# Kernel optimization log

Hardware: AMD Instinct MI355X
Metric: run time of the kernel (lower is better)

## Reference

```python
import jax, jax.numpy as jnp
import numpy as np
from jax import lax

PS = 8  # patch size

def setup_inputs() -> dict:
    key = jax.random.key(0)
    ks = jax.random.split(key, 7)
    dim = 64
    B, H, W = 4, 256, 256
    x = jax.random.normal(ks[0], (B, dim, H, W), dtype=jnp.float32)
    # to_hidden: Conv2d(dim, 6*dim, k=1)
    w_hidden = jax.random.normal(ks[1], (6 * dim, dim, 1, 1), dtype=jnp.float32) * 0.05
    b_hidden = jax.random.normal(ks[2], (6 * dim,), dtype=jnp.float32) * 0.01
    # to_hidden_dw: depthwise Conv2d(6*dim, 6*dim, k=3, pad=1, groups=6*dim)
    w_dw = jax.random.normal(ks[3], (6 * dim, 1, 3, 3), dtype=jnp.float32) * 0.05
    b_dw = jax.random.normal(ks[4], (6 * dim,), dtype=jnp.float32) * 0.01
    # project_out: Conv2d(2*dim, dim, k=1)
    w_out = jax.random.normal(ks[5], (dim, 2 * dim, 1, 1), dtype=jnp.float32) * 0.05
    b_out = jax.random.normal(ks[6], (dim,), dtype=jnp.float32) * 0.01
    return {"x": x, "w_hidden": w_hidden, "b_hidden": b_hidden,
            "w_dw": w_dw, "b_dw": b_dw, "w_out": w_out, "b_out": b_out}

def _conv(x, w, groups=1, padding='VALID'):
    return lax.conv_general_dilated(
        x, w, window_strides=(1, 1), padding=padding,
        dimension_numbers=('NCHW', 'OIHW', 'NCHW'),
        feature_group_count=groups)

def reference(x, w_hidden, b_hidden, w_dw, b_dw, w_out, b_out):
    # 1x1 expansion to 6*dim channels
    hidden = _conv(x, w_hidden) + b_hidden[None, :, None, None]
    # 3x3 depthwise conv (groups == channels)
    dw = _conv(hidden, w_dw, groups=w_dw.shape[0], padding='SAME') + b_dw[None, :, None, None]
    q, k, v = jnp.split(dw, 3, axis=1)  # each (B, 2*dim, H, W)
    B, C, H, W = q.shape
    # raw reshape into (B,C,H/8,W/8,8,8) exactly as torch .reshape on contiguous NCHW
    q_patch = q.reshape(B, C, H // PS, W // PS, PS, PS)
    k_patch = k.reshape(B, C, H // PS, W // PS, PS, PS)
    q_fft = jnp.fft.rfft2(q_patch)
    k_fft = jnp.fft.rfft2(k_patch)
    out = jnp.fft.irfft2(q_fft * k_fft, s=(PS, PS))  # circular conv of q,k patches
    out = out.reshape(B, C, (H // PS) * PS, (W // PS) * PS)
    output = v * out
    output = _conv(output, w_out) + b_out[None, :, None, None]
    return output
```

## Files before the change

kernel.cpp:

```cpp
#include <hip/hip_runtime.h>

#define HW 65536
#define W_IMG 256
#define H_IMG 256
#define CIN 64
#define CHID 384
#define CQK 128

__global__ __launch_bounds__(256) void k1_expand(
    const float* __restrict__ x_base,
    const float* __restrict__ wh,
    const float* __restrict__ bh,
    float* __restrict__ hidden_base,
    size_t x_bstride, size_t hid_bstride)
{
    const float* x = x_base + blockIdx.z * x_bstride;
    float* hidden  = hidden_base + blockIdx.z * hid_bstride;
    const int pxbase = blockIdx.x * 256;
    const int cobase = blockIdx.y * 64;
    const int tid  = threadIdx.x;
    const int lane = tid & 63;
    const int wq   = __builtin_amdgcn_readfirstlane(tid >> 6);
    const int px   = pxbase + lane * 4;
    const int cw   = cobase + wq * 16;

    float acc[16][4];
    #pragma unroll
    for (int i = 0; i < 16; ++i)
        #pragma unroll
        for (int j = 0; j < 4; ++j) acc[i][j] = 0.f;

    #pragma unroll 2
    for (int ci4 = 0; ci4 < CIN; ci4 += 4) {
        float4 xv[4];
        #pragma unroll
        for (int u = 0; u < 4; ++u)
            xv[u] = *reinterpret_cast<const float4*>(&x[(size_t)(ci4 + u) * HW + px]);
        #pragma unroll
        for (int i = 0; i < 16; ++i) {
            float4 wv = *reinterpret_cast<const float4*>(
                &wh[(size_t)(cw + i) * CIN + ci4]);
            float wu[4] = {wv.x, wv.y, wv.z, wv.w};
            #pragma unroll
            for (int u = 0; u < 4; ++u) {
                acc[i][0] += wu[u] * xv[u].x;
                acc[i][1] += wu[u] * xv[u].y;
                acc[i][2] += wu[u] * xv[u].z;
                acc[i][3] += wu[u] * xv[u].w;
            }
        }
    }

    #pragma unroll
    for (int i = 0; i < 16; ++i) {
        int co = cw + i;
        float b = bh[co];
        float4 o;
        o.x = acc[i][0] + b; o.y = acc[i][1] + b;
        o.z = acc[i][2] + b; o.w = acc[i][3] + b;
        *reinterpret_cast<float4*>(&hidden[(size_t)co * HW + px]) = o;
    }
}

__global__ __launch_bounds__(256) void k2_fused(
    const float* __restrict__ hidden_base,
    const float* __restrict__ wdw,
    const float* __restrict__ bdw,
    float* __restrict__ vout_base,
    size_t hid_bstride, size_t vout_bstride)
{
    __shared__ float stg[2][10][260];
    __shared__ float qk[2][8][4][68];

    const float* hidden = hidden_base + blockIdx.z * hid_bstride;
    float* vout         = vout_base + blockIdx.z * vout_bstride;

    const int c  = blockIdx.y;
    const int r0 = blockIdx.x * 8;
    const int tid = threadIdx.x;

    #pragma unroll
    for (int it = 0; it < 5; ++it) {
        int f4  = it * 256 + tid;
        int ch  = f4 / 640;
        int rem = f4 - ch * 640;
        int lr  = rem >> 6;
        int p4  = rem & 63;
        int gr  = r0 - 1 + lr;
        float4 v = make_float4(0.f, 0.f, 0.f, 0.f);
        if ((unsigned)gr < H_IMG)
            v = *reinterpret_cast<const float4*>(
                &hidden[(size_t)(c + ch * CQK) * HW + (size_t)gr * W_IMG + p4 * 4]);
        *reinterpret_cast<float4*>(&stg[ch][lr][p4 * 4]) = v;
    }
    __syncthreads();

    const int w = tid;
    const int segw = w >> 6;
    const int tw   = w & 63;
    #pragma unroll
    for (int ch = 0; ch < 2; ++ch) {
        const float* wv = wdw + (c + ch * CQK) * 9;
        const float bias = bdw[c + ch * CQK];
        const float w0 = wv[0], w1 = wv[1], w2 = wv[2];
        const float w3 = wv[3], w4 = wv[4], w5 = wv[5];
        const float w6 = wv[6], w7 = wv[7], w8 = wv[8];
        const float* S = &stg[ch][0][0];

        float am, a0, ap, bm, b0, bp;
        a0 = S[w];
        am = (w > 0)   ? S[w - 1] : 0.f;
        ap = (w < 255) ? S[w + 1] : 0.f;
        b0 = S[260 + w];
        bm = (w > 0)   ? S[260 + w - 1] : 0.f;
        bp = (w < 255) ? S[260 + w + 1] : 0.f;

        #pragma unroll
        for (int r = 0; r < 8; ++r) {
            const float* Sr = S + (r + 2) * 260;
            float c0 = Sr[w];
            float cm = (w > 0)   ? Sr[w - 1] : 0.f;
            float cp = (w < 255) ? Sr[w + 1] : 0.f;
            float a = bias + am * w0 + a0 * w1 + ap * w2
                           + bm * w3 + b0 * w4 + bp * w5
                           + cm * w6 + c0 * w7 + cp * w8;
            qk[ch][r][segw][tw] = a;
            am = bm; a0 = b0; ap = bp;
            bm = cm; b0 = c0; bp = cp;
        }
    }
    __syncthreads();

    const int row = tid >> 5;
    const int seg = (tid >> 3) & 3;
    const int i   = tid & 7;
    const int gr  = r0 + row;
    const int wp0 = seg * 64 + i * 8;

    const float* hbv = hidden + (size_t)(c + 2 * CQK) * HW;
    float4 hv[3][2];
    float  hm[3], hp[3];
    #pragma unroll
    for (int ky = 0; ky < 3; ++ky) {
        int grr = gr + ky - 1;
        hv[ky][0] = make_float4(0.f, 0.f, 0.f, 0.f);
        hv[ky][1] = make_float4(0.f, 0.f, 0.f, 0.f);
        hm[ky] = 0.f; hp[ky] = 0.f;
        if ((unsigned)grr < H_IMG) {
            const float* rb = hbv + (size_t)grr * W_IMG;
            hv[ky][0] = *reinterpret_cast<const float4*>(&rb[wp0]);
            hv[ky][1] = *reinterpret_cast<const float4*>(&rb[wp0 + 4]);
            hm[ky] = (wp0 > 0)   ? rb[wp0 - 1] : 0.f;
            hp[ky] = (wp0 < 248) ? rb[wp0 + 8] : 0.f;
        }
    }

    const float* qb = &qk[0][row][seg][0];
    const float* kb = &qk[1][row][seg][0];

    float acc[8];
    #pragma unroll
    for (int j = 0; j < 8; ++j) acc[j] = 0.f;

    #pragma unroll
    for (int s = 0; s < 8; ++s) {
        int qr = (i - s) & 7;
        float4 ka = *reinterpret_cast<const float4*>(&kb[s * 8]);
        float4 kc = *reinterpret_cast<const float4*>(&kb[s * 8 + 4]);
        float4 qa = *reinterpret_cast<const float4*>(&qb[qr * 8]);
        float4 qc = *reinterpret_cast<const float4*>(&qb[qr * 8 + 4]);
        float kr[8] = {ka.x, ka.y, ka.z, ka.w, kc.x, kc.y, kc.z, kc.w};
        float qv[8] = {qa.x, qa.y, qa.z, qa.w, qc.x, qc.y, qc.z, qc.w};
        #pragma unroll
        for (int t = 0; t < 8; ++t)
            #pragma unroll
            for (int j = 0; j < 8; ++j)
                acc[j] += kr[t] * qv[(j - t) & 7];
    }

    const float* wvv = wdw + (c + 2 * CQK) * 9;
    const float vbias = bdw[c + 2 * CQK];
    float vc[8];
    #pragma unroll
    for (int j = 0; j < 8; ++j) vc[j] = vbias;
    #pragma unroll
    for (int ky = 0; ky < 3; ++ky) {
        float kw0 = wvv[ky * 3], kw1 = wvv[ky * 3 + 1], kw2 = wvv[ky * 3 + 2];
        float h[10];
        h[0] = hm[ky];
        h[1] = hv[ky][0].x; h[2] = hv[ky][0].y; h[3] = hv[ky][0].z; h[4] = hv[ky][0].w;
        h[5] = hv[ky][1].x; h[6] = hv[ky][1].y; h[7] = hv[ky][1].z; h[8] = hv[ky][1].w;
        h[9] = hp[ky];
        #pragma unroll
        for (int j = 0; j < 8; ++j)
            vc[j] += h[j] * kw0 + h[j + 1] * kw1 + h[j + 2] * kw2;
    }

    float* dst = &vout[(size_t)c * HW + (size_t)gr * W_IMG + wp0];
    float4 o0, o1;
    o0.x = acc[0] * vc[0]; o0.y = acc[1] * vc[1];
    o0.z = acc[2] * vc[2]; o0.w = acc[3] * vc[3];
    o1.x = acc[4] * vc[4]; o1.y = acc[5] * vc[5];
    o1.z = acc[6] * vc[6]; o1.w = acc[7] * vc[7];
    *reinterpret_cast<float4*>(dst)     = o0;
    *reinterpret_cast<float4*>(dst + 4) = o1;
}

__global__ __launch_bounds__(256) void k3_project(
    const float* __restrict__ vout_base,
    const float* __restrict__ wo,
    const float* __restrict__ bo,
    float* __restrict__ out_base,
    size_t vout_bstride, size_t out_bstride)
{
    const float* vout = vout_base + blockIdx.z * vout_bstride;
    float* out        = out_base + blockIdx.z * out_bstride;
    const int pxbase = blockIdx.x * 256;
    const int tid  = threadIdx.x;
    const int lane = tid & 63;
    const int wq   = __builtin_amdgcn_readfirstlane(tid >> 6);
    const int px   = pxbase + lane * 4;
    const int cw   = wq * 16;

    float acc[16][4];
    #pragma unroll
    for (int i = 0; i < 16; ++i)
        #pragma unroll
        for (int j = 0; j < 4; ++j) acc[i][j] = 0.f;

    #pragma unroll 2
    for (int cc4 = 0; cc4 < CQK; cc4 += 4) {
        float4 xv[4];
        #pragma unroll
        for (int u = 0; u < 4; ++u)
            xv[u] = *reinterpret_cast<const float4*>(&vout[(size_t)(cc4 + u) * HW + px]);
        #pragma unroll
        for (int i = 0; i < 16; ++i) {
            float4 wv = *reinterpret_cast<const float4*>(
                &wo[(size_t)(cw + i) * CQK + cc4]);
            float wu[4] = {wv.x, wv.y, wv.z, wv.w};
            #pragma unroll
            for (int u = 0; u < 4; ++u) {
                acc[i][0] += wu[u] * xv[u].x;
                acc[i][1] += wu[u] * xv[u].y;
                acc[i][2] += wu[u] * xv[u].z;
                acc[i][3] += wu[u] * xv[u].w;
            }
        }
    }

    #pragma unroll
    for (int i = 0; i < 16; ++i) {
        int co = cw + i;
        float b = bo[co];
        float4 o;
        o.x = acc[i][0] + b; o.y = acc[i][1] + b;
        o.z = acc[i][2] + b; o.w = acc[i][3] + b;
        *reinterpret_cast<float4*>(&out[(size_t)co * HW + px]) = o;
    }
}

extern "C" void kernel_launch(void* const* d_in, const int* in_sizes, int n_in,
                              void* d_out, int out_size, void* d_ws, size_t ws_size,
                              hipStream_t stream) {
    const float* x   = (const float*)d_in[0];
    const float* wh  = (const float*)d_in[1];
    const float* bh  = (const float*)d_in[2];
    const float* wdw = (const float*)d_in[3];
    const float* bdw = (const float*)d_in[4];
    const float* wo  = (const float*)d_in[5];
    const float* bo  = (const float*)d_in[6];
    float* out = (float*)d_out;

    const size_t n_hid  = (size_t)CHID * HW;
    const size_t n_vout = (size_t)CQK * HW;
    const size_t n_x    = (size_t)CIN * HW;

    if (ws_size >= 4 * (n_hid + n_vout) * sizeof(float)) {
        float* hidden = (float*)d_ws;
        float* vout   = hidden + 4 * n_hid;
        k1_expand <<<dim3(HW / 256, CHID / 64, 4), 256, 0, stream>>>(
            x, wh, bh, hidden, n_x, n_hid);
        k2_fused  <<<dim3(H_IMG / 8, CQK, 4),      256, 0, stream>>>(
            hidden, wdw, bdw, vout, n_hid, n_vout);
        k3_project<<<dim3(HW / 256, 1, 4),         256, 0, stream>>>(
            vout, wo, bo, out, n_vout, n_x);
    } else {
        float* hidden = (float*)d_ws;
        float* vout   = hidden + n_hid;
        for (int b = 0; b < 4; ++b) {
            const float* xb = x + (size_t)b * n_x;
            float* ob       = out + (size_t)b * n_x;
            k1_expand <<<dim3(HW / 256, CHID / 64, 1), 256, 0, stream>>>(
                xb, wh, bh, hidden, 0, 0);
            k2_fused  <<<dim3(H_IMG / 8, CQK, 1),      256, 0, stream>>>(
                hidden, wdw, bdw, vout, 0, 0);
            k3_project<<<dim3(HW / 256, 1, 1),         256, 0, stream>>>(
                vout, wo, bo, ob, 0, 0);
        }
    }
}
```

Before: 420.1 us.

## Shrink channel tiles in 1x1 convs and restage depthwise conv one channel at a time

k1_expand now computes 32 output channels per block instead of 64, and k3_project splits its 64 outputs across four blocks of 16. Both changes raise the block count and cut per-thread accumulator registers, which should help occupancy. The price is re-reading the input pixels more times. k2_fused now stages one q/k channel at a time into a smaller padded shared buffer with zero halo columns, which removes the boundary branches, and it issues the v-halo loads before the depthwise stage. This lowers LDS use but adds a sync between the two channels.

Result: faster. 407.5 us (-3.0%).

```diff
diff --git a/kernel.cpp b/kernel.cpp
--- a/kernel.cpp
+++ b/kernel.cpp
@@ -17,16 +17,16 @@
     const float* x = x_base + blockIdx.z * x_bstride;
     float* hidden  = hidden_base + blockIdx.z * hid_bstride;
     const int pxbase = blockIdx.x * 256;
-    const int cobase = blockIdx.y * 64;
+    const int cobase = blockIdx.y * 32;
     const int tid  = threadIdx.x;
     const int lane = tid & 63;
     const int wq   = __builtin_amdgcn_readfirstlane(tid >> 6);
     const int px   = pxbase + lane * 4;
-    const int cw   = cobase + wq * 16;
-
-    float acc[16][4];
-    #pragma unroll
-    for (int i = 0; i < 16; ++i)
+    const int cw   = cobase + wq * 8;
+
+    float acc[8][4];
+    #pragma unroll
+    for (int i = 0; i < 8; ++i)
         #pragma unroll
         for (int j = 0; j < 4; ++j) acc[i][j] = 0.f;
 
@@ -37,7 +37,7 @@
         for (int u = 0; u < 4; ++u)
             xv[u] = *reinterpret_cast<const float4*>(&x[(size_t)(ci4 + u) * HW + px]);
         #pragma unroll
-        for (int i = 0; i < 16; ++i) {
+        for (int i = 0; i < 8; ++i) {
             float4 wv = *reinterpret_cast<const float4*>(
                 &wh[(size_t)(cw + i) * CIN + ci4]);
             float wu[4] = {wv.x, wv.y, wv.z, wv.w};
@@ -52,7 +52,7 @@
     }
 
     #pragma unroll
-    for (int i = 0; i < 16; ++i) {
+    for (int i = 0; i < 8; ++i) {
         int co = cw + i;
         float b = bh[co];
         float4 o;
@@ -69,7 +69,7 @@
     float* __restrict__ vout_base,
     size_t hid_bstride, size_t vout_bstride)
 {
-    __shared__ float stg[2][10][260];
+    __shared__ float stg[10 * 264];
     __shared__ float qk[2][8][4][68];
 
     const float* hidden = hidden_base + blockIdx.z * hid_bstride;
@@ -78,58 +78,6 @@
     const int c  = blockIdx.y;
     const int r0 = blockIdx.x * 8;
     const int tid = threadIdx.x;
-
-    #pragma unroll
-    for (int it = 0; it < 5; ++it) {
-        int f4  = it * 256 + tid;
-        int ch  = f4 / 640;
-        int rem = f4 - ch * 640;
-        int lr  = rem >> 6;
-        int p4  = rem & 63;
-        int gr  = r0 - 1 + lr;
-        float4 v = make_float4(0.f, 0.f, 0.f, 0.f);
-        if ((unsigned)gr < H_IMG)
-            v = *reinterpret_cast<const float4*>(
-                &hidden[(size_t)(c + ch * CQK) * HW + (size_t)gr * W_IMG + p4 * 4]);
-        *reinterpret_cast<float4*>(&stg[ch][lr][p4 * 4]) = v;
-    }
-    __syncthreads();
-
-    const int w = tid;
-    const int segw = w >> 6;
-    const int tw   = w & 63;
-    #pragma unroll
-    for (int ch = 0; ch < 2; ++ch) {
-        const float* wv = wdw + (c + ch * CQK) * 9;
-        const float bias = bdw[c + ch * CQK];
-        const float w0 = wv[0], w1 = wv[1], w2 = wv[2];
-        const float w3 = wv[3], w4 = wv[4], w5 = wv[5];
-        const float w6 = wv[6], w7 = wv[7], w8 = wv[8];
-        const float* S = &stg[ch][0][0];
-
-        float am, a0, ap, bm, b0, bp;
-        a0 = S[w];
-        am = (w > 0)   ? S[w - 1] : 0.f;
-        ap = (w < 255) ? S[w + 1] : 0.f;
-        b0 = S[260 + w];
-        bm = (w > 0)   ? S[260 + w - 1] : 0.f;
-        bp = (w < 255) ? S[260 + w + 1] : 0.f;
-
-        #pragma unroll
-        for (int r = 0; r < 8; ++r) {
-            const float* Sr = S + (r + 2) * 260;
-            float c0 = Sr[w];
-            float cm = (w > 0)   ? Sr[w - 1] : 0.f;
-            float cp = (w < 255) ? Sr[w + 1] : 0.f;
-            float a = bias + am * w0 + a0 * w1 + ap * w2
-                           + bm * w3 + b0 * w4 + bp * w5
-                           + cm * w6 + c0 * w7 + cp * w8;
-            qk[ch][r][segw][tw] = a;
-            am = bm; a0 = b0; ap = bp;
-            bm = cm; b0 = c0; bp = cp;
-        }
-    }
-    __syncthreads();
 
     const int row = tid >> 5;
     const int seg = (tid >> 3) & 3;
@@ -155,6 +103,56 @@
         }
     }
 
+    const int w = tid;
+    const int segw = w >> 6;
+    const int tw   = w & 63;
+
+    #pragma unroll
+    for (int ch = 0; ch < 2; ++ch) {
+        if (ch) __syncthreads();
+        #pragma unroll
+        for (int it = 0; it < 3; ++it) {
+            int f4 = it * 256 + tid;
+            if (f4 < 640) {
+                int lr = f4 >> 6;
+                int p4 = f4 & 63;
+                int grr = r0 - 1 + lr;
+                float4 v = make_float4(0.f, 0.f, 0.f, 0.f);
+                if ((unsigned)grr < H_IMG)
+                    v = *reinterpret_cast<const float4*>(
+                        &hidden[(size_t)(c + ch * CQK) * HW + (size_t)grr * W_IMG + p4 * 4]);
+                *reinterpret_cast<float4*>(&stg[lr * 264 + 4 + p4 * 4]) = v;
+            }
+        }
+        if (tid < 10) {
+            stg[tid * 264 + 3]   = 0.f;
+            stg[tid * 264 + 260] = 0.f;
+        }
+        __syncthreads();
+
+        const float* wv = wdw + (c + ch * CQK) * 9;
+        const float bias = bdw[c + ch * CQK];
+        const float w0 = wv[0], w1 = wv[1], w2 = wv[2];
+        const float w3 = wv[3], w4 = wv[4], w5 = wv[5];
+        const float w6 = wv[6], w7 = wv[7], w8 = wv[8];
+
+        const float* S0 = &stg[w + 3];
+        float am = S0[0],       a0 = S0[1],       ap = S0[2];
+        float bm = S0[264],     b0 = S0[265],     bp = S0[266];
+        #pragma unroll
+        for (int r = 0; r < 8; ++r) {
+            const float* Sr = S0 + (r + 2) * 264;
+            float cm = Sr[0], c0 = Sr[1], cp = Sr[2];
+            float a = bias + am * w0 + a0 * w1 + ap * w2
+                           + bm * w3 + b0 * w4 + bp * w5
+                           + cm * w6 + c0 * w7 + cp * w8;
+            qk[ch][r][segw][tw] = a;
+            am = bm; a0 = b0; ap = bp;
+            bm = cm; b0 = c0; bp = cp;
+        }
+    }
+    __syncthreads();
+
     const float* qb = &qk[0][row][seg][0];
     const float* kb = &qk[1][row][seg][0];
 
@@ -216,15 +214,16 @@
     const float* vout = vout_base + blockIdx.z * vout_bstride;
     float* out        = out_base + blockIdx.z * out_bstride;
     const int pxbase = blockIdx.x * 256;
+    const int cobase = blockIdx.y * 16;
     const int tid  = threadIdx.x;
     const int lane = tid & 63;
     const int wq   = __builtin_amdgcn_readfirstlane(tid >> 6);
     const int px   = pxbase + lane * 4;
-    const int cw   = wq * 16;
-
-    float acc[16][4];
-    #pragma unroll
-    for (int i = 0; i < 16; ++i)
+    const int cw   = cobase + wq * 4;
+
+    float acc[4][4];
+    #pragma unroll
+    for (int i = 0; i < 4; ++i)
         #pragma unroll
         for (int j = 0; j < 4; ++j) acc[i][j] = 0.f;
 
@@ -235,7 +234,7 @@
         for (int u = 0; u < 4; ++u)
             xv[u] = *reinterpret_cast<const float4*>(&vout[(size_t)(cc4 + u) * HW + px]);
         #pragma unroll
-        for (int i = 0; i < 16; ++i) {
+        for (int i = 0; i < 4; ++i) {
             float4 wv = *reinterpret_cast<const float4*>(
                 &wo[(size_t)(cw + i) * CQK + cc4]);
             float wu[4] = {wv.x, wv.y, wv.z, wv.w};
@@ -250,7 +249,7 @@
     }
 
     #pragma unroll
-    for (int i = 0; i < 16; ++i) {
+    for (int i = 0; i < 4; ++i) {
         int co = cw + i;
         float b = bo[co];
         float4 o;
@@ -279,11 +278,11 @@
     if (ws_size >= 4 * (n_hid + n_vout) * sizeof(float)) {
         float* hidden = (float*)d_ws;
         float* vout   = hidden + 4 * n_hid;
-        k1_expand <<<dim3(HW / 256, CHID / 64, 4), 256, 0, stream>>>(
+        k1_expand <<<dim3(HW / 256, CHID / 32, 4), 256, 0, stream>>>(
             x, wh, bh, hidden, n_x, n_hid);
         k2_fused  <<<dim3(H_IMG / 8, CQK, 4),      256, 0, stream>>>(
             hidden, wdw, bdw, vout, n_hid, n_vout);
-        k3_project<<<dim3(HW / 256, 1, 4),         256, 0, stream>>>(
+        k3_project<<<dim3(HW / 256, 64 / 16, 4),   256, 0, stream>>>(
             vout, wo, bo, out, n_vout, n_x);
     } else {
         float* hidden = (float*)d_ws;
@@ -291,11 +290,11 @@
         for (int b = 0; b < 4; ++b) {
             const float* xb = x + (size_t)b * n_x;
             float* ob       = out + (size_t)b * n_x;
-            k1_expand <<<dim3(HW / 256, CHID / 64, 1), 256, 0, stream>>>(
+            k1_expand <<<dim3(HW / 256, CHID / 32, 1), 256, 0, stream>>>(
                 xb, wh, bh, hidden, 0, 0);
             k2_fused  <<<dim3(H_IMG / 8, CQK, 1),      256, 0, stream>>>(
                 hidden, wdw, bdw, vout, 0, 0);
-            k3_project<<<dim3(HW / 256, 1, 1),         256, 0, stream>>>(
+            k3_project<<<dim3(HW / 256, 64 / 16, 1),   256, 0, stream>>>(
                 vout, wo, bo, ob, 0, 0);
         }
     }
```
